# Kernel optimization log

Hardware: AMD Instinct MI355X
Metric: run time of the kernel (lower is better)

The kernel has to match this reference:

```python
import jax, jax.numpy as jnp
import numpy as np

# Fixed-shape Conformer chunked attention (Gemma3n audio style)
S = 8192          # seq_len
H = 16            # num_heads
D = 128           # head_dim
HD = H * D        # hidden size = 2048
C = 12            # chunk_size
MP = 12           # max_past_horizon
MF = 0            # max_future_horizon
CTX = C + MP + MF # context_size = 24
POS = MP + MF + 1 # pos_length = 13
N = (S + C - 1) // C            # num_blocks
PAD = N * C - S                 # pad_amount
Q_SCALE = D ** -0.5 * 1.4426950408889634  # head_dim**-0.5 / softplus(0)
SOFTCAP = 50.0


def setup_inputs() -> dict:
    key = jax.random.key(0)
    ks = jax.random.split(key, 8)
    w = lambda k, shape: jax.random.normal(k, shape, jnp.float32) * 0.02
    return {
        "hidden_states": jax.random.normal(ks[0], (1, S, HD), jnp.float32),
        "position_embeddings": jax.random.normal(ks[1], (POS, HD), jnp.float32),
        "Wq": w(ks[2], (HD, HD)),
        "Wk": w(ks[3], (HD, HD)),
        "Wv": w(ks[4], (HD, HD)),
        "W_rel": w(ks[5], (HD, HD)),
        "W_post": w(ks[6], (HD, HD)),
        "per_dim_scale": jax.random.normal(ks[7], (D,), jnp.float32) * 0.1,
    }


def reference(hidden_states, position_embeddings, Wq, Wk, Wv, W_rel, W_post, per_dim_scale):
    x = hidden_states[0]  # [S, HD]
    q = (x @ Wq).reshape(S, H, D) * (Q_SCALE * jax.nn.softplus(per_dim_scale))
    k = (x @ Wk).reshape(S, H, D)  # k_scale = 1.0
    v = (x @ Wv).reshape(S, H, D)

    # query blocks [N, C, H, D]
    qb = jnp.pad(q, ((0, PAD), (0, 0), (0, 0))).reshape(N, C, H, D)
    # key/value padded then gathered into sliding context blocks [N, CTX, H, D]
    kp = jnp.pad(k, ((MP, MF + C - 1), (0, 0), (0, 0)))
    vp = jnp.pad(v, ((MP, MF + C - 1), (0, 0), (0, 0)))
    idx = jnp.arange(N)[:, None] * C + jnp.arange(CTX)[None, :]  # [N, CTX]
    kb = kp[idx]
    vb = vp[idx]

    rel_k = (position_embeddings @ W_rel).reshape(POS, H, D)

    # content scores [H, N, C, CTX]
    ac = jnp.einsum('nchd,nkhd->hnck', qb, kb)
    # relative-position scores via shift trick
    bd = jnp.einsum('nchd,phd->hncp', qb, rel_k)          # [H, N, C, POS]
    bd = jnp.pad(bd, ((0, 0), (0, 0), (0, 0), (0, CTX + 1 - POS)))
    bd = bd.reshape(H, N, C * (CTX + 1))[:, :, :C * CTX].reshape(H, N, C, CTX)

    attn = jnp.tanh((ac + bd) / SOFTCAP) * SOFTCAP        # softcap
    attn = jax.nn.softmax(attn, axis=-1)

    out = jnp.einsum('hnck,nkhd->nchd', attn, vb).reshape(N * C, HD)[:S]
    return (out @ W_post)[None]  # [1, S, HD]
```

## Files before the change

kernel.cpp:

```cpp
#include <hip/hip_runtime.h>
#include <hip/hip_bf16.h>

#define S_LEN 8192
#define NH    16
#define HD    128
#define HID   2048
#define NQKV  6144
#define CHUNK 12
#define MP    12
#define CTX   24
#define POS   13
#define NBLK  683

typedef short bf16x8 __attribute__((ext_vector_type(8)));
typedef float f32x4  __attribute__((ext_vector_type(4)));
typedef unsigned short u16;
typedef u16 u16x8 __attribute__((ext_vector_type(8)));
typedef u16 u16x4 __attribute__((ext_vector_type(4)));

#define MFMA16 __builtin_amdgcn_mfma_f32_16x16x32_bf16

__device__ __forceinline__ void glds16(const u16* g, u16* l) {
  __builtin_amdgcn_global_load_lds(
      (__attribute__((address_space(1))) void*)(void*)g,
      (__attribute__((address_space(3))) void*)l, 16, 0, 0);
}

__device__ __forceinline__ u16 f2b(float f) {
  __hip_bfloat16 h = __float2bfloat16(f);
  return *(u16*)&h;
}

__global__ __launch_bounds__(256) void f32_to_bf16(const float* __restrict__ in,
                                                   u16* __restrict__ out, int n) {
  int i = (blockIdx.x * 256 + threadIdx.x) * 4;
  if (i < n) {
    float4 v = *(const float4*)(in + i);
    u16x4 o = {f2b(v.x), f2b(v.y), f2b(v.z), f2b(v.w)};
    *(u16x4*)(out + i) = o;
  }
}

__global__ __launch_bounds__(256) void transpose4(const float* __restrict__ W0,
                                                  const float* __restrict__ W1,
                                                  const float* __restrict__ W2,
                                                  const float* __restrict__ W3,
                                                  u16* __restrict__ out) {
  __shared__ u16 t[64][72];
  const int z = blockIdx.z;
  const float* in = (z == 0) ? W0 : (z == 1) ? W1 : (z == 2) ? W2 : W3;
  u16* dst = out + (size_t)z * HID * HID;
  const int bx = blockIdx.x * 64, by = blockIdx.y * 64;
  const int x = threadIdx.x & 63;
  const int y4 = threadIdx.x >> 6;
  for (int r = y4; r < 64; r += 4)
    t[r][x] = f2b(in[(size_t)(by + r) * HID + bx + x]);
  __syncthreads();
  for (int r = y4; r < 64; r += 4)
    dst[(size_t)(bx + r) * HID + by + x] = t[x][r];
}

__global__ void qscale_kernel(const float* __restrict__ pds, float* __restrict__ qs) {
  int d = threadIdx.x;
  float x = pds[d];
  float sp = log1pf(expf(x));
  qs[d] = 0.08838834764831845f * 1.4426950408889634f * sp;
}

__global__ __launch_bounds__(256) void relk_atomic(const float* __restrict__ pos,
                                                   const float* __restrict__ Wrel,
                                                   float* __restrict__ RELF) {
  const int col = blockIdx.x * 256 + threadIdx.x;
  const int c0 = blockIdx.y * 256;
  float acc[POS] = {};
  for (int c = c0; c < c0 + 256; ++c) {
    float wv = Wrel[(size_t)c * HID + col];
#pragma unroll
    for (int p = 0; p < POS; ++p) acc[p] += pos[p * HID + c] * wv;
  }
#pragma unroll
  for (int p = 0; p < POS; ++p) atomicAdd(&RELF[p * HID + col], acc[p]);
}

__global__ __launch_bounds__(256) void relk_cvt(const float* __restrict__ RELF,
                                                u16* __restrict__ REL) {
  int i = blockIdx.x * 256 + threadIdx.x;
  if (i < POS * HID) REL[i] = f2b(RELF[i]);
}

#define BMT 256
#define BNT 256
#define BKT 32
#define NT  (HID / BKT)

__global__ __launch_bounds__(512, 2) void gemm_bt(const u16* __restrict__ A,
                                                  const u16* __restrict__ Bt,
                                                  u16* __restrict__ Co,
                                                  float* __restrict__ Cf,
                                                  const float* __restrict__ colscale,
                                                  int NN, int csLimit) {
  __shared__ u16 lds[4][2][BMT * BKT];
  const int tid = threadIdx.x;
  const int lane = tid & 63, w = tid >> 6;
  const int quad = lane >> 4, l = lane & 15;
  const int wm = (w >> 2) * 128, wn = (w & 3) * 64;

  const int orig = blockIdx.y * gridDim.x + blockIdx.x;
  const int xcd = orig & 7, k = orig >> 3;
  const int bm = (xcd * 4 + (k & 3)) * BMT;
  const int bn = (k >> 2) * BNT;

  const int rdoff = (l >> 1) * 64 + (((((l & 1) << 2) | quad)) ^ ((l >> 1) & 7)) * 8;

  const int sl = (lane & 7) ^ (lane >> 3);
  const int srow = ((lane >> 3) << 1) + (sl >> 2);
  const int sk = (sl & 3) * 8;
  const u16* Ag0 = A + (size_t)(bm + w * 32 + srow) * HID + sk;
  const u16* Ag1 = Ag0 + (size_t)16 * HID;
  const u16* Bg0 = Bt + (size_t)(bn + w * 32 + srow) * HID + sk;
  const u16* Bg1 = Bg0 + (size_t)16 * HID;

  f32x4 acc[8][4] = {};

#pragma unroll
  for (int pt = 0; pt < 3; ++pt) {
    u16* sA = &lds[pt][0][w * 1024];
    u16* sB = &lds[pt][1][w * 1024];
    glds16(Ag0 + pt * BKT, sA);
    glds16(Ag1 + pt * BKT, sA + 512);
    glds16(Bg0 + pt * BKT, sB);
    glds16(Bg1 + pt * BKT, sB + 512);
  }
  asm volatile("s_waitcnt vmcnt(8)" ::: "memory");
  __builtin_amdgcn_s_barrier();

  bf16x8 afC[4], bfC[4], afN[4], bfN[4];
#pragma unroll
  for (int i = 0; i < 4; ++i)
    afC[i] = *(const bf16x8*)(&lds[0][0][0] + (wm + i * 16) * 32 + rdoff);
#pragma unroll
  for (int j = 0; j < 4; ++j)
    bfC[j] = *(const bf16x8*)(&lds[0][1][0] + (wn + j * 16) * 32 + rdoff);

#pragma unroll 1
  for (int t = 0; t < NT; ++t) {
    const u16* bufA = &lds[t & 3][0][0];
    u16* stA = &lds[(t + 3) & 3][0][w * 1024];
    u16* stB = &lds[(t + 3) & 3][1][w * 1024];
    const int kt = (t + 3) * BKT;
    const bool doStage = (t < NT - 3);

    if (doStage) {
      glds16(Ag0 + kt, stA);
      glds16(Ag1 + kt, stA + 512);
    }
    bf16x8 af1[4];
#pragma unroll
    for (int i = 0; i < 4; ++i)
      af1[i] = *(const bf16x8*)(bufA + (wm + 64 + i * 16) * 32 + rdoff);
    asm volatile("s_waitcnt lgkmcnt(4)" ::: "memory");
    __builtin_amdgcn_sched_barrier(0);
    __builtin_amdgcn_s_setprio(1);
#pragma unroll
    for (int i = 0; i < 4; ++i)
#pragma unroll
      for (int j = 0; j < 4; ++j)
        acc[i][j] = MFMA16(afC[i], bfC[j], acc[i][j], 0, 0, 0);
    __builtin_amdgcn_s_setprio(0);

    if (doStage) {
      glds16(Bg0 + kt, stB);
      glds16(Bg1 + kt, stB + 512);
    }
    asm volatile("s_waitcnt lgkmcnt(0)" ::: "memory");
    if (t < NT - 3)       asm volatile("s_waitcnt vmcnt(8)" ::: "memory");
    else if (t == NT - 3) asm volatile("s_waitcnt vmcnt(4)" ::: "memory");
    else if (t == NT - 2) asm volatile("s_waitcnt vmcnt(0)" ::: "memory");
    __builtin_amdgcn_sched_barrier(0);
    if (t < NT - 1) {
      __builtin_amdgcn_s_barrier();
      const u16* nA = &lds[(t + 1) & 3][0][0];
      const u16* nB = &lds[(t + 1) & 3][1][0];
#pragma unroll
      for (int i = 0; i < 4; ++i)
        afN[i] = *(const bf16x8*)(nA + (wm + i * 16) * 32 + rdoff);
#pragma unroll
      for (int j = 0; j < 4; ++j)
        bfN[j] = *(const bf16x8*)(nB + (wn + j * 16) * 32 + rdoff);
    }
    __builtin_amdgcn_s_setprio(1);
#pragma unroll
    for (int i = 0; i < 4; ++i)
#pragma unroll
      for (int j = 0; j < 4; ++j)
        acc[4 + i][j] = MFMA16(af1[i], bfC[j], acc[4 + i][j], 0, 0, 0);
    __builtin_amdgcn_s_setprio(0);
#pragma unroll
    for (int r = 0; r < 4; ++r) {
      afC[r] = afN[r];
      bfC[r] = bfN[r];
    }
  }

#pragma unroll
  for (int i = 0; i < 8; ++i)
#pragma unroll
    for (int j = 0; j < 4; ++j)
#pragma unroll
      for (int r = 0; r < 4; ++r) {
        int row = bm + wm + i * 16 + quad * 4 + r;
        int col = bn + wn + j * 16 + l;
        float v = acc[i][j][r];
        if (colscale && col < csLimit) v *= colscale[col & (HD - 1)];
        if (Cf) Cf[(size_t)row * NN + col] = v;
        else    Co[(size_t)row * NN + col] = f2b(v);
      }
}

__global__ __launch_bounds__(64, 4) void attn_kernel(const u16* __restrict__ qkv,
                                                     const u16* __restrict__ relg,
                                                     u16* __restrict__ og) {
  __shared__ u16 vt[128 * 32];
  __shared__ u16 ps[16 * 32];
  const int n = blockIdx.x, h = blockIdx.y;
  const int lane = threadIdx.x;
  const int quad = lane >> 4, l = lane & 15;
  const int base = n * CHUNK;
  const u16x8 zero8 = {0, 0, 0, 0, 0, 0, 0, 0};

  const u16* qg = qkv + h * HD;
  const u16* kg = qkv + 2048 + h * HD;
  const u16* vg = qkv + 4096 + h * HD;

  u16x8 vld[8];
#pragma unroll
  for (int i = 0; i < 8; ++i) {
    int id = lane + 64 * i;
    int ctx = id & 31, dc = id >> 5;
    int s = base + ctx - MP;
    vld[i] = (ctx < CTX && s >= 0 && s < S_LEN)
                 ? *(const u16x8*)(vg + (size_t)s * NQKV + dc * 8)
                 : zero8;
  }

  const bool qv = (l < CHUNK) && (base + l < S_LEN);
  const bool k0v = (base + l - MP) >= 0;
  const bool k1v = (l < 8) && (base + 4 + l < S_LEN);
  const u16* qrow = qg + (size_t)(base + l) * NQKV;
  const u16* k0row = kg + (size_t)(base + l - MP) * NQKV;
  const u16* k1row = kg + (size_t)(base + 4 + l) * NQKV;

  bf16x8 aQf[4], bK0f[4], bK1f[4];
#pragma unroll
  for (int t = 0; t < 4; ++t) {
    int d0 = t * 32 + quad * 8;
    aQf[t] = qv ? *(const bf16x8*)(qrow + d0) : (bf16x8)zero8;
    bK0f[t] = k0v ? *(const bf16x8*)(k0row + d0) : (bf16x8)zero8;
    bK1f[t] = k1v ? *(const bf16x8*)(k1row + d0) : (bf16x8)zero8;
  }

  f32x4 ac0 = {0, 0, 0, 0}, ac1 = {0, 0, 0, 0}, bd = {0, 0, 0, 0};
#pragma unroll
  for (int t = 0; t < 4; ++t) {
    int d0 = t * 32;
    bf16x8 bR = (bf16x8)zero8;
    if (l < POS)
      bR = *(const bf16x8*)(relg + (size_t)l * HID + h * HD + d0 + quad * 8);
    ac0 = MFMA16(aQf[t], bK0f[t], ac0, 0, 0, 0);
    ac1 = MFMA16(aQf[t], bK1f[t], ac1, 0, 0, 0);
    bd = MFMA16(aQf[t], bR, bd, 0, 0, 0);
  }

  float p0[4], p1[4];
#pragma unroll
  for (int r = 0; r < 4; ++r) {
    int c = quad * 4 + r;
    int pi0 = l - c;
    int pi1 = 16 + l - c;
    int sp0 = pi0 < 0 ? 0 : (pi0 > 15 ? 15 : pi0);
    int sp1 = pi1 < 0 ? 0 : (pi1 > 15 ? 15 : pi1);
    float b0 = __shfl(bd[r], quad * 16 + sp0, 64);
    float b1 = __shfl(bd[r], quad * 16 + sp1, 64);
    b0 = (pi0 >= 0 && pi0 < POS) ? b0 : 0.0f;
    b1 = (pi1 >= 0 && pi1 < POS) ? b1 : 0.0f;
    float s0 = tanhf((ac0[r] + b0) * (1.0f / 50.0f)) * 50.0f;
    float s1 = tanhf((ac1[r] + b1) * (1.0f / 50.0f)) * 50.0f;
    bool v1 = (l < (CTX - 16));
    if (!v1) s1 = -1e30f;
    float mx = fmaxf(s0, s1);
#pragma unroll
    for (int d = 1; d < 16; d <<= 1) mx = fmaxf(mx, __shfl_xor(mx, d, 64));
    float e0 = __expf(s0 - mx);
    float e1 = v1 ? __expf(s1 - mx) : 0.0f;
    float sm = e0 + e1;
#pragma unroll
    for (int d = 1; d < 16; d <<= 1) sm += __shfl_xor(sm, d, 64);
    float inv = 1.0f / sm;
    p0[r] = e0 * inv;
    p1[r] = e1 * inv;
  }

#pragma unroll
  for (int i = 0; i < 8; ++i) {
    int id = lane + 64 * i;
    int ctx = id & 31, dc = id >> 5;
#pragma unroll
    for (int jj = 0; jj < 8; ++jj) {
      int d = dc * 8 + jj;
      int fq = (d >> 1) & 3;
      vt[d * 32 + (((ctx >> 3) ^ fq) << 3) + (ctx & 7)] = vld[i][jj];
    }
  }
#pragma unroll
  for (int r = 0; r < 4; ++r) {
    int c = quad * 4 + r;
    int fc = (c >> 1) & 3;
    ps[c * 32 + (((l >> 3) ^ fc) << 3) + (l & 7)] = f2b(p0[r]);
    ps[c * 32 + ((((16 + l) >> 3) ^ fc) << 3) + (l & 7)] = f2b(p1[r]);
  }
  __syncthreads();

  const int fl = (l >> 1) & 3;
  bf16x8 aP = *(const bf16x8*)(ps + l * 32 + ((quad ^ fl) << 3));
#pragma unroll
  for (int nt = 0; nt < 8; ++nt) {
    int d = nt * 16 + l;
    bf16x8 bV = *(const bf16x8*)(vt + d * 32 + ((quad ^ fl) << 3));
    f32x4 o = {0, 0, 0, 0};
    o = MFMA16(aP, bV, o, 0, 0, 0);
#pragma unroll
    for (int r = 0; r < 4; ++r) {
      int c = quad * 4 + r;
      int s = base + c;
      if (c < CHUNK && s < S_LEN)
        og[(size_t)s * HID + h * HD + nt * 16 + l] = f2b(o[r]);
    }
  }
}

extern "C" void kernel_launch(void* const* d_in, const int* in_sizes, int n_in,
                              void* d_out, int out_size, void* d_ws, size_t ws_size,
                              hipStream_t stream) {
  const float* x = (const float*)d_in[0];
  const float* pos = (const float*)d_in[1];
  const float* Wq = (const float*)d_in[2];
  const float* Wk = (const float*)d_in[3];
  const float* Wv = (const float*)d_in[4];
  const float* Wrel = (const float*)d_in[5];
  const float* Wpost = (const float*)d_in[6];
  const float* pds = (const float*)d_in[7];

  char* ws = (char*)d_ws;
  u16* WT  = (u16*)(ws);
  u16* xb  = (u16*)(ws + 33554432);
  u16* AO  = xb;
  u16* QKV = (u16*)(ws + 67108864);
  float* RELF = (float*)(ws + 167772160);
  u16* REL = (u16*)(ws + 167878656);
  float* QS = (float*)(ws + 167931904);

  const int NX = S_LEN * HID;
  f32_to_bf16<<<NX / 4 / 256, 256, 0, stream>>>(x, xb, NX);

  transpose4<<<dim3(32, 32, 4), 256, 0, stream>>>(Wq, Wk, Wv, Wpost, WT);
  qscale_kernel<<<1, 128, 0, stream>>>(pds, QS);

  hipMemsetAsync(RELF, 0, POS * HID * sizeof(float), stream);
  relk_atomic<<<dim3(8, 8), 256, 0, stream>>>(pos, Wrel, RELF);
  relk_cvt<<<(POS * HID + 255) / 256, 256, 0, stream>>>(RELF, REL);

  gemm_bt<<<dim3(32, 24), 512, 0, stream>>>(xb, WT, QKV, nullptr, QS, NQKV, 2048);

  attn_kernel<<<dim3(NBLK, NH), 64, 0, stream>>>(QKV, REL, AO);

  gemm_bt<<<dim3(32, 8), 512, 0, stream>>>(AO, WT + (size_t)3 * HID * HID,
                                           nullptr, (float*)d_out, nullptr, HID, 0);
}
```

Measured before the change: 556.0 us.

## Process eight chunks per attention wave with double-buffered register prefetch

```diff
diff --git a/kernel.cpp b/kernel.cpp
--- a/kernel.cpp
+++ b/kernel.cpp
@@ -11,6 +11,7 @@
 #define CTX   24
 #define POS   13
 #define NBLK  683
+#define NCPW  8
 
 typedef short bf16x8 __attribute__((ext_vector_type(8)));
 typedef float f32x4  __attribute__((ext_vector_type(4)));
@@ -29,6 +30,11 @@
 __device__ __forceinline__ u16 f2b(float f) {
   __hip_bfloat16 h = __float2bfloat16(f);
   return *(u16*)&h;
+}
+
+__device__ __forceinline__ float tanh_fast(float x) {
+  float e2 = __expf(x + x);
+  return 1.0f - 2.0f / (e2 + 1.0f);
 }
 
 __global__ __launch_bounds__(256) void f32_to_bf16(const float* __restrict__ in,
@@ -217,123 +223,149 @@
       }
 }
 
-__global__ __launch_bounds__(64, 4) void attn_kernel(const u16* __restrict__ qkv,
+__global__ __launch_bounds__(64, 2) void attn_kernel(const u16* __restrict__ qkv,
                                                      const u16* __restrict__ relg,
                                                      u16* __restrict__ og) {
   __shared__ u16 vt[128 * 32];
   __shared__ u16 ps[16 * 32];
-  const int n = blockIdx.x, h = blockIdx.y;
+  const int n0 = blockIdx.x * NCPW, h = blockIdx.y;
   const int lane = threadIdx.x;
   const int quad = lane >> 4, l = lane & 15;
-  const int base = n * CHUNK;
   const u16x8 zero8 = {0, 0, 0, 0, 0, 0, 0, 0};
 
   const u16* qg = qkv + h * HD;
   const u16* kg = qkv + 2048 + h * HD;
   const u16* vg = qkv + 4096 + h * HD;
 
-  u16x8 vld[8];
-#pragma unroll
-  for (int i = 0; i < 8; ++i) {
-    int id = lane + 64 * i;
-    int ctx = id & 31, dc = id >> 5;
-    int s = base + ctx - MP;
-    vld[i] = (ctx < CTX && s >= 0 && s < S_LEN)
-                 ? *(const u16x8*)(vg + (size_t)s * NQKV + dc * 8)
-                 : zero8;
-  }
-
-  const bool qv = (l < CHUNK) && (base + l < S_LEN);
-  const bool k0v = (base + l - MP) >= 0;
-  const bool k1v = (l < 8) && (base + 4 + l < S_LEN);
-  const u16* qrow = qg + (size_t)(base + l) * NQKV;
-  const u16* k0row = kg + (size_t)(base + l - MP) * NQKV;
-  const u16* k1row = kg + (size_t)(base + 4 + l) * NQKV;
-
-  bf16x8 aQf[4], bK0f[4], bK1f[4];
-#pragma unroll
-  for (int t = 0; t < 4; ++t) {
-    int d0 = t * 32 + quad * 8;
-    aQf[t] = qv ? *(const bf16x8*)(qrow + d0) : (bf16x8)zero8;
-    bK0f[t] = k0v ? *(const bf16x8*)(k0row + d0) : (bf16x8)zero8;
-    bK1f[t] = k1v ? *(const bf16x8*)(k1row + d0) : (bf16x8)zero8;
-  }
-
-  f32x4 ac0 = {0, 0, 0, 0}, ac1 = {0, 0, 0, 0}, bd = {0, 0, 0, 0};
-#pragma unroll
-  for (int t = 0; t < 4; ++t) {
-    int d0 = t * 32;
-    bf16x8 bR = (bf16x8)zero8;
-    if (l < POS)
-      bR = *(const bf16x8*)(relg + (size_t)l * HID + h * HD + d0 + quad * 8);
-    ac0 = MFMA16(aQf[t], bK0f[t], ac0, 0, 0, 0);
-    ac1 = MFMA16(aQf[t], bK1f[t], ac1, 0, 0, 0);
-    bd = MFMA16(aQf[t], bR, bd, 0, 0, 0);
-  }
-
-  float p0[4], p1[4];
-#pragma unroll
-  for (int r = 0; r < 4; ++r) {
-    int c = quad * 4 + r;
-    int pi0 = l - c;
-    int pi1 = 16 + l - c;
-    int sp0 = pi0 < 0 ? 0 : (pi0 > 15 ? 15 : pi0);
-    int sp1 = pi1 < 0 ? 0 : (pi1 > 15 ? 15 : pi1);
-    float b0 = __shfl(bd[r], quad * 16 + sp0, 64);
-    float b1 = __shfl(bd[r], quad * 16 + sp1, 64);
-    b0 = (pi0 >= 0 && pi0 < POS) ? b0 : 0.0f;
-    b1 = (pi1 >= 0 && pi1 < POS) ? b1 : 0.0f;
-    float s0 = tanhf((ac0[r] + b0) * (1.0f / 50.0f)) * 50.0f;
-    float s1 = tanhf((ac1[r] + b1) * (1.0f / 50.0f)) * 50.0f;
-    bool v1 = (l < (CTX - 16));
-    if (!v1) s1 = -1e30f;
-    float mx = fmaxf(s0, s1);
-#pragma unroll
-    for (int d = 1; d < 16; d <<= 1) mx = fmaxf(mx, __shfl_xor(mx, d, 64));
-    float e0 = __expf(s0 - mx);
-    float e1 = v1 ? __expf(s1 - mx) : 0.0f;
-    float sm = e0 + e1;
-#pragma unroll
-    for (int d = 1; d < 16; d <<= 1) sm += __shfl_xor(sm, d, 64);
-    float inv = 1.0f / sm;
-    p0[r] = e0 * inv;
-    p1[r] = e1 * inv;
-  }
-
-#pragma unroll
-  for (int i = 0; i < 8; ++i) {
-    int id = lane + 64 * i;
-    int ctx = id & 31, dc = id >> 5;
-#pragma unroll
-    for (int jj = 0; jj < 8; ++jj) {
-      int d = dc * 8 + jj;
-      int fq = (d >> 1) & 3;
-      vt[d * 32 + (((ctx >> 3) ^ fq) << 3) + (ctx & 7)] = vld[i][jj];
-    }
-  }
-#pragma unroll
-  for (int r = 0; r < 4; ++r) {
-    int c = quad * 4 + r;
-    int fc = (c >> 1) & 3;
-    ps[c * 32 + (((l >> 3) ^ fc) << 3) + (l & 7)] = f2b(p0[r]);
-    ps[c * 32 + ((((16 + l) >> 3) ^ fc) << 3) + (l & 7)] = f2b(p1[r]);
-  }
-  __syncthreads();
-
-  const int fl = (l >> 1) & 3;
-  bf16x8 aP = *(const bf16x8*)(ps + l * 32 + ((quad ^ fl) << 3));
-#pragma unroll
-  for (int nt = 0; nt < 8; ++nt) {
-    int d = nt * 16 + l;
-    bf16x8 bV = *(const bf16x8*)(vt + d * 32 + ((quad ^ fl) << 3));
-    f32x4 o = {0, 0, 0, 0};
-    o = MFMA16(aP, bV, o, 0, 0, 0);
+  bf16x8 bRf[4];
+#pragma unroll
+  for (int t = 0; t < 4; ++t)
+    bRf[t] = (l < POS)
+                 ? *(const bf16x8*)(relg + (size_t)l * HID + h * HD + t * 32 + quad * 8)
+                 : (bf16x8)zero8;
+
+  u16x8 vldA[8], vldB[8];
+  bf16x8 aQfA[4], bK0fA[4], bK1fA[4];
+  bf16x8 aQfB[4], bK0fB[4], bK1fB[4];
+
+  auto PF = [&](u16x8 (&vld)[8], bf16x8 (&aQf)[4], bf16x8 (&bK0f)[4],
+                bf16x8 (&bK1f)[4], int n) {
+    if (n >= NBLK) return;
+    const int base = n * CHUNK;
+#pragma unroll
+    for (int i = 0; i < 8; ++i) {
+      int id = lane + 64 * i;
+      int ctx = id & 31, dc = id >> 5;
+      int s = base + ctx - MP;
+      vld[i] = (ctx < CTX && s >= 0 && s < S_LEN)
+                   ? *(const u16x8*)(vg + (size_t)s * NQKV + dc * 8)
+                   : zero8;
+    }
+    const bool qv = (l < CHUNK) && (base + l < S_LEN);
+    const bool k0v = (base + l - MP) >= 0;
+    const bool k1v = (l < 8) && (base + 4 + l < S_LEN);
+    const u16* qrow = qg + (size_t)(base + l) * NQKV;
+    const u16* k0row = kg + (size_t)(base + l - MP) * NQKV;
+    const u16* k1row = kg + (size_t)(base + 4 + l) * NQKV;
+#pragma unroll
+    for (int t = 0; t < 4; ++t) {
+      int d0 = t * 32 + quad * 8;
+      aQf[t] = qv ? *(const bf16x8*)(qrow + d0) : (bf16x8)zero8;
+      bK0f[t] = k0v ? *(const bf16x8*)(k0row + d0) : (bf16x8)zero8;
+      bK1f[t] = k1v ? *(const bf16x8*)(k1row + d0) : (bf16x8)zero8;
+    }
+  };
+
+  auto CMP = [&](u16x8 (&vld)[8], bf16x8 (&aQf)[4], bf16x8 (&bK0f)[4],
+                 bf16x8 (&bK1f)[4], int n) {
+    if (n >= NBLK) return;
+    const int base = n * CHUNK;
+
+    f32x4 ac0 = {0, 0, 0, 0}, ac1 = {0, 0, 0, 0}, bd = {0, 0, 0, 0};
+#pragma unroll
+    for (int t = 0; t < 4; ++t) {
+      ac0 = MFMA16(aQf[t], bK0f[t], ac0, 0, 0, 0);
+      ac1 = MFMA16(aQf[t], bK1f[t], ac1, 0, 0, 0);
+      bd = MFMA16(aQf[t], bRf[t], bd, 0, 0, 0);
+    }
+
+    float p0[4], p1[4];
 #pragma unroll
     for (int r = 0; r < 4; ++r) {
       int c = quad * 4 + r;
-      int s = base + c;
-      if (c < CHUNK && s < S_LEN)
-        og[(size_t)s * HID + h * HD + nt * 16 + l] = f2b(o[r]);
+      int pi0 = l - c;
+      int pi1 = 16 + l - c;
+      int sp0 = pi0 < 0 ? 0 : (pi0 > 15 ? 15 : pi0);
+      int sp1 = pi1 < 0 ? 0 : (pi1 > 15 ? 15 : pi1);
+      float b0 = __shfl(bd[r], quad * 16 + sp0, 64);
+      float b1 = __shfl(bd[r], quad * 16 + sp1, 64);
+      b0 = (pi0 >= 0 && pi0 < POS) ? b0 : 0.0f;
+      b1 = (pi1 >= 0 && pi1 < POS) ? b1 : 0.0f;
+      float s0 = tanh_fast((ac0[r] + b0) * (1.0f / 50.0f)) * 50.0f;
+      float s1 = tanh_fast((ac1[r] + b1) * (1.0f / 50.0f)) * 50.0f;
+      bool v1 = (l < (CTX - 16));
+      if (!v1) s1 = -1e30f;
+      float mx = fmaxf(s0, s1);
+#pragma unroll
+      for (int d = 1; d < 16; d <<= 1) mx = fmaxf(mx, __shfl_xor(mx, d, 64));
+      float e0 = __expf(s0 - mx);
+      float e1 = v1 ? __expf(s1 - mx) : 0.0f;
+      float sm = e0 + e1;
+#pragma unroll
+      for (int d = 1; d < 16; d <<= 1) sm += __shfl_xor(sm, d, 64);
+      float inv = 1.0f / sm;
+      p0[r] = e0 * inv;
+      p1[r] = e1 * inv;
+    }
+
+    __syncthreads();
+#pragma unroll
+    for (int i = 0; i < 8; ++i) {
+      int id = lane + 64 * i;
+      int ctx = id & 31, dc = id >> 5;
+#pragma unroll
+      for (int jj = 0; jj < 8; ++jj) {
+        int d = dc * 8 + jj;
+        int fq = (d >> 1) & 3;
+        vt[d * 32 + (((ctx >> 3) ^ fq) << 3) + (ctx & 7)] = vld[i][jj];
+      }
+    }
+#pragma unroll
+    for (int r = 0; r < 4; ++r) {
+      int c = quad * 4 + r;
+      int fc = (c >> 1) & 3;
+      ps[c * 32 + (((l >> 3) ^ fc) << 3) + (l & 7)] = f2b(p0[r]);
+      ps[c * 32 + ((((16 + l) >> 3) ^ fc) << 3) + (l & 7)] = f2b(p1[r]);
+    }
+    __syncthreads();
+
+    const int fl = (l >> 1) & 3;
+    bf16x8 aP = *(const bf16x8*)(ps + l * 32 + ((quad ^ fl) << 3));
+#pragma unroll
+    for (int nt = 0; nt < 8; ++nt) {
+      int d = nt * 16 + l;
+      bf16x8 bV = *(const bf16x8*)(vt + d * 32 + ((quad ^ fl) << 3));
+      f32x4 o = {0, 0, 0, 0};
+      o = MFMA16(aP, bV, o, 0, 0, 0);
+#pragma unroll
+      for (int r = 0; r < 4; ++r) {
+        int c = quad * 4 + r;
+        int s = base + c;
+        if (c < CHUNK && s < S_LEN)
+          og[(size_t)s * HID + h * HD + nt * 16 + l] = f2b(o[r]);
+      }
+    }
+  };
+
+  PF(vldA, aQfA, bK0fA, bK1fA, n0);
+#pragma unroll
+  for (int cc = 0; cc < NCPW; ++cc) {
+    if ((cc & 1) == 0) {
+      if (cc < NCPW - 1) PF(vldB, aQfB, bK0fB, bK1fB, n0 + cc + 1);
+      CMP(vldA, aQfA, bK0fA, bK1fA, n0 + cc);
+    } else {
+      if (cc < NCPW - 1) PF(vldA, aQfA, bK0fA, bK1fA, n0 + cc + 1);
+      CMP(vldB, aQfB, bK0fB, bK1fB, n0 + cc);
     }
   }
 }
@@ -371,7 +403,7 @@
 
   gemm_bt<<<dim3(32, 24), 512, 0, stream>>>(xb, WT, QKV, nullptr, QS, NQKV, 2048);
 
-  attn_kernel<<<dim3(NBLK, NH), 64, 0, stream>>>(QKV, REL, AO);
+  attn_kernel<<<dim3((NBLK + NCPW - 1) / NCPW, NH), 64, 0, stream>>>(QKV, REL, AO);
 
   gemm_bt<<<dim3(32, 8), 512, 0, stream>>>(AO, WT + (size_t)3 * HID * HID,
                                            nullptr, (float*)d_out, nullptr, HID, 0);
```

Result: slower. 662.4 us (+19.1%).
